# Optimization experiments

Hardware: AMD Instinct MI355X
Metric: run time of the kernel (lower is better)

The kernel has to match this reference:

```python
import jax, jax.numpy as jnp
import numpy as np

QMIN, QMAX = 0, 255        # 8-bit asymmetric activation quant bounds
GROUP_SIZE = 128

def setup_inputs() -> dict:
    key = jax.random.key(0)
    k1, k2, k3, k4, k5 = jax.random.split(key, 5)
    x = jax.random.normal(k1, (1, 2048, 4096), dtype=jnp.float32)
    qweight = jax.random.randint(k2, (4096, 32, 128), 0, 16, dtype=jnp.int32)  # uint4 codes
    w_scales = jax.random.uniform(k3, (4096, 32), dtype=jnp.float32, minval=0.001, maxval=0.02)
    w_zero_points = jax.random.randint(k4, (4096, 32), 0, 16, dtype=jnp.int32)
    bias = jax.random.normal(k5, (4096,), dtype=jnp.float32)
    return {"x": x, "qweight": qweight, "w_scales": w_scales,
            "w_zero_points": w_zero_points, "bias": bias}

def reference(x, qweight, w_scales, w_zero_points, bias):
    xf = x.astype(jnp.float32)
    # per-token (last-dim) asymmetric dynamic activation quantization
    xmin = jnp.min(xf, axis=-1, keepdims=True)
    xmax = jnp.max(xf, axis=-1, keepdims=True)
    x_scale = jnp.clip((xmax - xmin) / (QMAX - QMIN), 1e-5, None)
    x_zp = jnp.clip(jnp.round(-xmin / x_scale), QMIN, QMAX)
    q = jnp.clip(jnp.round(xf / x_scale) + x_zp, QMIN, QMAX)
    centered_x = (q - x_zp).reshape(*x.shape[:-1], -1, GROUP_SIZE)  # [B,S,G,C]
    # grouped weight dequant (zero-point centered)
    centered_w = qweight.astype(jnp.float32) - w_zero_points.astype(jnp.float32)[..., None]  # [O,G,C]
    acc = jnp.einsum('bsgc,ogc->bsog', centered_x, centered_w)  # [B,S,O,G]
    out = (acc * w_scales[None, None]).sum(axis=-1)  # apply per-group weight scales
    out = out * x_scale  # per-token activation scale
    out = out + bias
    return out
```

## Files before the change

kernel.cpp:

```cpp
#include <hip/hip_runtime.h>
#include <hip/hip_bf16.h>
#include <stdint.h>

#define M_DIM 2048
#define N_DIM 4096
#define K_DIM 4096
#define NGROUP 32
#define GSIZE 128

#define BM 128
#define BN 64
#define BKB 128

typedef __attribute__((ext_vector_type(4))) int   int32x4_t;
typedef __attribute__((ext_vector_type(4))) float f32x4_t;

static __device__ __forceinline__ void gl2lds16(const void* g, void* l) {
    auto gp = (const __attribute__((address_space(1))) unsigned int*)(uintptr_t)g;
    auto lp = (__attribute__((address_space(3))) unsigned int*)(uintptr_t)l;
    __builtin_amdgcn_global_load_lds(gp, lp, 16, 0, 0);
}

#define QUANT_BLOCKS M_DIM
#define DEQ_BLOCKS ((N_DIM * K_DIM) / 8 / 256)
#define WT_BLOCKS ((N_DIM * NGROUP) / 256)

__global__ __launch_bounds__(256) void prep_kernel(
        const float* __restrict__ x,
        const int* __restrict__ qw,
        const float* __restrict__ wsc,
        const int* __restrict__ wzp,
        char* __restrict__ A8,
        char* __restrict__ Bt8,
        float* __restrict__ xscale,
        float* __restrict__ xzpc,
        float* __restrict__ WS,
        float* __restrict__ wsct)
{
    const int t = threadIdx.x;
    if (blockIdx.x < QUANT_BLOCKS) {
        const int s = blockIdx.x;
        const float* xrow = x + (size_t)s * K_DIM;

        float xv[16];
        float vmin = 1e38f, vmax = -1e38f;
#pragma unroll
        for (int p = 0; p < 4; ++p) {
            float4 v = *((const float4*)(xrow + p * 1024) + t);
            xv[p*4+0] = v.x; xv[p*4+1] = v.y; xv[p*4+2] = v.z; xv[p*4+3] = v.w;
            vmin = fminf(vmin, fminf(fminf(v.x, v.y), fminf(v.z, v.w)));
            vmax = fmaxf(vmax, fmaxf(fmaxf(v.x, v.y), fmaxf(v.z, v.w)));
        }
#pragma unroll
        for (int off = 32; off > 0; off >>= 1) {
            vmin = fminf(vmin, __shfl_xor(vmin, off));
            vmax = fmaxf(vmax, __shfl_xor(vmax, off));
        }
        __shared__ float smin[4], smax[4];
        const int wave = t >> 6;
        if ((t & 63) == 0) { smin[wave] = vmin; smax[wave] = vmax; }
        __syncthreads();
        vmin = fminf(fminf(smin[0], smin[1]), fminf(smin[2], smin[3]));
        vmax = fmaxf(fmaxf(smax[0], smax[1]), fmaxf(smax[2], smax[3]));

        float sc = (vmax - vmin) / 255.0f;
        sc = fmaxf(sc, 1e-5f);
        float zp = rintf(-vmin / sc);
        zp = fminf(fmaxf(zp, 0.0f), 255.0f);

#pragma unroll
        for (int p = 0; p < 4; ++p) {
            int b[4];
#pragma unroll
            for (int e = 0; e < 4; ++e) {
                float q = fminf(fmaxf(rintf(xv[p*4+e] / sc) + zp, 0.0f), 255.0f);
                b[e] = (int)q - 128;
            }
            unsigned pack = (b[0] & 0xff) | ((b[1] & 0xff) << 8) |
                            ((b[2] & 0xff) << 16) | ((b[3] & 0xff) << 24);
            *(unsigned*)(A8 + (size_t)s * K_DIM + p * 1024 + t * 4) = pack;
        }
        if (t == 0) { xscale[s] = sc; xzpc[s] = 128.0f - zp; }
    } else if (blockIdx.x < QUANT_BLOCKS + DEQ_BLOCKS) {
        const size_t base = ((size_t)(blockIdx.x - QUANT_BLOCKS) * 256 + t) * 8;
        const int n = (int)(base >> 12);
        const int g = (int)((base >> 7) & 31);
        const int zp = wzp[n * NGROUP + g];

        int4 c0 = *(const int4*)(qw + base);
        int4 c1 = *(const int4*)(qw + base + 4);
        int v0 = c0.x - zp, v1 = c0.y - zp, v2 = c0.z - zp, v3 = c0.w - zp;
        int v4 = c1.x - zp, v5 = c1.y - zp, v6 = c1.z - zp, v7 = c1.w - zp;
        uint2 pk;
        pk.x = (v0 & 0xff) | ((v1 & 0xff) << 8) | ((v2 & 0xff) << 16) | ((v3 & 0xff) << 24);
        pk.y = (v4 & 0xff) | ((v5 & 0xff) << 8) | ((v6 & 0xff) << 16) | ((v7 & 0xff) << 24);
        *(uint2*)(Bt8 + base) = pk;

        int s8 = v0 + v1 + v2 + v3 + v4 + v5 + v6 + v7;
#pragma unroll
        for (int off = 1; off < 16; off <<= 1) s8 += __shfl_xor(s8, off);
        if ((t & 15) == 0)
            atomicAdd(WS + n, wsc[n * NGROUP + g] * (float)s8);
    } else {
        const int idx = (blockIdx.x - QUANT_BLOCKS - DEQ_BLOCKS) * 256 + t;
        const int n = idx >> 5, g = idx & 31;
        wsct[g * N_DIM + n] = wsc[idx];
    }
}

__global__ __launch_bounds__(256, 4) void gemm_kernel(
        const char* __restrict__ A8,
        const char* __restrict__ Bt8,
        const float* __restrict__ xscale,
        const float* __restrict__ xzpc,
        const float* __restrict__ wsct,
        const float* __restrict__ WS,
        const float* __restrict__ bias,
        float* __restrict__ out)
{
    __shared__ __align__(16) char As[BM * BKB];
    __shared__ __align__(16) char Bs[BN * BKB];

    const int tid  = threadIdx.x;
    const int bm   = blockIdx.y;
    const int bn   = blockIdx.x;
    const int wave = tid >> 6;
    const int lane = tid & 63;
    const int wr   = (wave >> 1) * 64;
    const int wc   = (wave & 1) * 32;
    const int lrow  = lane & 15;
    const int lquad = lane >> 4;
    const int l7    = lrow & 7;

    const int srow8 = lane >> 3;
    const int cdat  = (lane & 7) ^ srow8;

    int32x4_t iacc[4][2];
    f32x4_t   facc[4][2];
    const int32x4_t zi = {0, 0, 0, 0};
    const f32x4_t   zf = {0.f, 0.f, 0.f, 0.f};
#pragma unroll
    for (int i = 0; i < 4; ++i)
#pragma unroll
        for (int j = 0; j < 2; ++j) { iacc[i][j] = zi; facc[i][j] = zf; }

    const char* Ab = A8  + (size_t)(bm * BM) * K_DIM;
    const char* Bb = Bt8 + (size_t)(bn * BN) * K_DIM;

    for (int kt = 0; kt < K_DIM / GSIZE; ++kt) {
        const int k0 = kt * GSIZE;
        __syncthreads();
#pragma unroll
        for (int p = 0; p < 4; ++p) {
            const int rbase = (p * 4 + wave) * 8;
            gl2lds16(Ab + (size_t)(rbase + srow8) * K_DIM + k0 + cdat * 16,
                     As + rbase * BKB);
        }
#pragma unroll
        for (int p = 0; p < 2; ++p) {
            const int rbase = (p * 4 + wave) * 8;
            gl2lds16(Bb + (size_t)(rbase + srow8) * K_DIM + k0 + cdat * 16,
                     Bs + rbase * BKB);
        }
        __syncthreads();

#pragma unroll
        for (int ks = 0; ks < 2; ++ks) {
            const int kc = ks * 4 + lquad;
            int32x4_t af[4], bf[2];
#pragma unroll
            for (int i = 0; i < 4; ++i)
                af[i] = *(const int32x4_t*)(As + (wr + i * 16 + lrow) * BKB + ((kc ^ l7) * 16));
#pragma unroll
            for (int j = 0; j < 2; ++j)
                bf[j] = *(const int32x4_t*)(Bs + (wc + j * 16 + lrow) * BKB + ((kc ^ l7) * 16));
#pragma unroll
            for (int i = 0; i < 4; ++i)
#pragma unroll
                for (int j = 0; j < 2; ++j)
                    iacc[i][j] = __builtin_amdgcn_mfma_i32_16x16x64_i8(
                        af[i], bf[j], iacc[i][j], 0, 0, 0);
        }

#pragma unroll
        for (int j = 0; j < 2; ++j) {
            const int n = bn * BN + wc + j * 16 + lrow;
            const float scl = wsct[kt * N_DIM + n];
#pragma unroll
            for (int i = 0; i < 4; ++i) {
#pragma unroll
                for (int r = 0; r < 4; ++r)
                    facc[i][j][r] += scl * (float)iacc[i][j][r];
                iacc[i][j] = zi;
            }
        }
    }

    const int m0 = bm * BM + wr;
    const int n0 = bn * BN + wc;
    float wsn[2], bn2[2];
#pragma unroll
    for (int j = 0; j < 2; ++j) {
        const int n = n0 + j * 16 + lrow;
        wsn[j] = WS[n]; bn2[j] = bias[n];
    }
#pragma unroll
    for (int i = 0; i < 4; ++i) {
#pragma unroll
        for (int r = 0; r < 4; ++r) {
            const int m = m0 + i * 16 + lquad * 4 + r;
            const float xs = xscale[m];
            const float czp = xzpc[m];
#pragma unroll
            for (int j = 0; j < 2; ++j) {
                const int n = n0 + j * 16 + lrow;
                out[(size_t)m * N_DIM + n] = xs * (facc[i][j][r] + czp * wsn[j]) + bn2[j];
            }
        }
    }
}

extern "C" void kernel_launch(void* const* d_in, const int* in_sizes, int n_in,
                              void* d_out, int out_size, void* d_ws, size_t ws_size,
                              hipStream_t stream) {
    const float* x     = (const float*)d_in[0];
    const int*   qw    = (const int*)d_in[1];
    const float* wsc   = (const float*)d_in[2];
    const int*   wzp   = (const int*)d_in[3];
    const float* bias  = (const float*)d_in[4];
    float* out = (float*)d_out;

    char* A8  = (char*)d_ws;
    char* Bt8 = A8 + (size_t)M_DIM * K_DIM;
    float* xscale = (float*)(Bt8 + (size_t)N_DIM * K_DIM);
    float* xzpc   = xscale + M_DIM;
    float* WS     = xzpc + M_DIM;
    float* wsct   = WS + N_DIM;

    hipMemsetAsync(WS, 0, N_DIM * sizeof(float), stream);
    prep_kernel<<<QUANT_BLOCKS + DEQ_BLOCKS + WT_BLOCKS, 256, 0, stream>>>(
        x, qw, wsc, wzp, A8, Bt8, xscale, xzpc, WS, wsct);
    dim3 grid(N_DIM / BN, M_DIM / BM);
    gemm_kernel<<<grid, 256, 0, stream>>>(A8, Bt8, xscale, xzpc, wsct, WS, bias, out);
}
```

Measured before the change: 202.0 us.

## Enlarge GEMM tile to 128x128x256 with 32x32 int8 MFMA and LDS scales

```diff
diff --git a/kernel.cpp b/kernel.cpp
--- a/kernel.cpp
+++ b/kernel.cpp
@@ -9,11 +9,12 @@
 #define GSIZE 128
 
 #define BM 128
-#define BN 64
-#define BKB 128
-
-typedef __attribute__((ext_vector_type(4))) int   int32x4_t;
-typedef __attribute__((ext_vector_type(4))) float f32x4_t;
+#define BN 128
+#define BKB 256
+
+typedef __attribute__((ext_vector_type(4)))  int   int32x4_t;
+typedef __attribute__((ext_vector_type(16))) int   int32x16_t;
+typedef __attribute__((ext_vector_type(16))) float f32x16_t;
 
 static __device__ __forceinline__ void gl2lds16(const void* g, void* l) {
     auto gp = (const __attribute__((address_space(1))) unsigned int*)(uintptr_t)g;
@@ -23,7 +24,6 @@
 
 #define QUANT_BLOCKS M_DIM
 #define DEQ_BLOCKS ((N_DIM * K_DIM) / 8 / 256)
-#define WT_BLOCKS ((N_DIM * NGROUP) / 256)
 
 __global__ __launch_bounds__(256) void prep_kernel(
         const float* __restrict__ x,
@@ -34,8 +34,7 @@
         char* __restrict__ Bt8,
         float* __restrict__ xscale,
         float* __restrict__ xzpc,
-        float* __restrict__ WS,
-        float* __restrict__ wsct)
+        float* __restrict__ WS)
 {
     const int t = threadIdx.x;
     if (blockIdx.x < QUANT_BLOCKS) {
@@ -81,7 +80,7 @@
             *(unsigned*)(A8 + (size_t)s * K_DIM + p * 1024 + t * 4) = pack;
         }
         if (t == 0) { xscale[s] = sc; xzpc[s] = 128.0f - zp; }
-    } else if (blockIdx.x < QUANT_BLOCKS + DEQ_BLOCKS) {
+    } else {
         const size_t base = ((size_t)(blockIdx.x - QUANT_BLOCKS) * 256 + t) * 8;
         const int n = (int)(base >> 12);
         const int g = (int)((base >> 7) & 31);
@@ -101,25 +100,22 @@
         for (int off = 1; off < 16; off <<= 1) s8 += __shfl_xor(s8, off);
         if ((t & 15) == 0)
             atomicAdd(WS + n, wsc[n * NGROUP + g] * (float)s8);
-    } else {
-        const int idx = (blockIdx.x - QUANT_BLOCKS - DEQ_BLOCKS) * 256 + t;
-        const int n = idx >> 5, g = idx & 31;
-        wsct[g * N_DIM + n] = wsc[idx];
-    }
-}
-
-__global__ __launch_bounds__(256, 4) void gemm_kernel(
+    }
+}
+
+__global__ __launch_bounds__(256, 2) void gemm_kernel(
         const char* __restrict__ A8,
         const char* __restrict__ Bt8,
         const float* __restrict__ xscale,
         const float* __restrict__ xzpc,
-        const float* __restrict__ wsct,
+        const float* __restrict__ wsc,
         const float* __restrict__ WS,
         const float* __restrict__ bias,
         float* __restrict__ out)
 {
     __shared__ __align__(16) char As[BM * BKB];
     __shared__ __align__(16) char Bs[BN * BKB];
+    __shared__ float Ssc[NGROUP * BN];
 
     const int tid  = threadIdx.x;
     const int bm   = blockIdx.y;
@@ -127,94 +123,107 @@
     const int wave = tid >> 6;
     const int lane = tid & 63;
     const int wr   = (wave >> 1) * 64;
-    const int wc   = (wave & 1) * 32;
-    const int lrow  = lane & 15;
-    const int lquad = lane >> 4;
-    const int l7    = lrow & 7;
-
-    const int srow8 = lane >> 3;
-    const int cdat  = (lane & 7) ^ srow8;
-
-    int32x4_t iacc[4][2];
-    f32x4_t   facc[4][2];
-    const int32x4_t zi = {0, 0, 0, 0};
-    const f32x4_t   zf = {0.f, 0.f, 0.f, 0.f};
-#pragma unroll
-    for (int i = 0; i < 4; ++i)
-#pragma unroll
-        for (int j = 0; j < 2; ++j) { iacc[i][j] = zi; facc[i][j] = zf; }
+    const int wc   = (wave & 1) * 64;
+    const int l31  = lane & 31;
+    const int hi   = lane >> 5;
+    const int l7   = l31 & 7;
+
+    const int n0 = bn * BN;
+    {
+        const int n = tid >> 1, gh = (tid & 1) * 16;
+        const float4* src = (const float4*)(wsc + (size_t)(n0 + n) * NGROUP + gh);
+#pragma unroll
+        for (int j4 = 0; j4 < 4; ++j4) {
+            float4 v = src[j4];
+            Ssc[(gh + j4 * 4 + 0) * BN + n] = v.x;
+            Ssc[(gh + j4 * 4 + 1) * BN + n] = v.y;
+            Ssc[(gh + j4 * 4 + 2) * BN + n] = v.z;
+            Ssc[(gh + j4 * 4 + 3) * BN + n] = v.w;
+        }
+    }
+
+    int32x16_t iacc[2][2];
+    f32x16_t   facc[2][2];
+    int32x16_t ZERO;
+#pragma unroll
+    for (int r = 0; r < 16; ++r) ZERO[r] = 0;
+#pragma unroll
+    for (int i = 0; i < 2; ++i)
+#pragma unroll
+        for (int j = 0; j < 2; ++j) {
+            iacc[i][j] = ZERO;
+#pragma unroll
+            for (int r = 0; r < 16; ++r) facc[i][j][r] = 0.0f;
+        }
 
     const char* Ab = A8  + (size_t)(bm * BM) * K_DIM;
     const char* Bb = Bt8 + (size_t)(bn * BN) * K_DIM;
 
-    for (int kt = 0; kt < K_DIM / GSIZE; ++kt) {
-        const int k0 = kt * GSIZE;
+    const int srow4 = lane >> 4;
+
+    for (int kt = 0; kt < K_DIM / BKB; ++kt) {
+        const int k0 = kt * BKB;
         __syncthreads();
 #pragma unroll
-        for (int p = 0; p < 4; ++p) {
-            const int rbase = (p * 4 + wave) * 8;
-            gl2lds16(Ab + (size_t)(rbase + srow8) * K_DIM + k0 + cdat * 16,
-                     As + rbase * BKB);
-        }
-#pragma unroll
-        for (int p = 0; p < 2; ++p) {
-            const int rbase = (p * 4 + wave) * 8;
-            gl2lds16(Bb + (size_t)(rbase + srow8) * K_DIM + k0 + cdat * 16,
-                     Bs + rbase * BKB);
+        for (int p = 0; p < 8; ++p) {
+            const int rbase = (p * 4 + wave) * 4;
+            const int r = rbase + srow4;
+            const int cdat = (lane & 15) ^ (r & 7);
+            gl2lds16(Ab + (size_t)r * K_DIM + k0 + cdat * 16, As + rbase * BKB);
+            gl2lds16(Bb + (size_t)r * K_DIM + k0 + cdat * 16, Bs + rbase * BKB);
         }
         __syncthreads();
 
 #pragma unroll
-        for (int ks = 0; ks < 2; ++ks) {
-            const int kc = ks * 4 + lquad;
-            int32x4_t af[4], bf[2];
-#pragma unroll
-            for (int i = 0; i < 4; ++i)
-                af[i] = *(const int32x4_t*)(As + (wr + i * 16 + lrow) * BKB + ((kc ^ l7) * 16));
-#pragma unroll
-            for (int j = 0; j < 2; ++j)
-                bf[j] = *(const int32x4_t*)(Bs + (wc + j * 16 + lrow) * BKB + ((kc ^ l7) * 16));
-#pragma unroll
-            for (int i = 0; i < 4; ++i)
+        for (int half = 0; half < 2; ++half) {
+            const int g = kt * 2 + half;
+            float scl[2];
+            scl[0] = Ssc[g * BN + wc + 0  + l31];
+            scl[1] = Ssc[g * BN + wc + 32 + l31];
+
+#pragma unroll
+            for (int ks4 = 0; ks4 < 4; ++ks4) {
+                const int ks = half * 4 + ks4;
+                const int cc = ks * 2 + hi;
+                int32x4_t af[2], bf[2];
+#pragma unroll
+                for (int i = 0; i < 2; ++i)
+                    af[i] = *(const int32x4_t*)(As + (wr + i * 32 + l31) * BKB + ((cc ^ l7) * 16));
 #pragma unroll
                 for (int j = 0; j < 2; ++j)
-                    iacc[i][j] = __builtin_amdgcn_mfma_i32_16x16x64_i8(
-                        af[i], bf[j], iacc[i][j], 0, 0, 0);
-        }
-
-#pragma unroll
-        for (int j = 0; j < 2; ++j) {
-            const int n = bn * BN + wc + j * 16 + lrow;
-            const float scl = wsct[kt * N_DIM + n];
-#pragma unroll
-            for (int i = 0; i < 4; ++i) {
-#pragma unroll
-                for (int r = 0; r < 4; ++r)
-                    facc[i][j][r] += scl * (float)iacc[i][j][r];
-                iacc[i][j] = zi;
+                    bf[j] = *(const int32x4_t*)(Bs + (wc + j * 32 + l31) * BKB + ((cc ^ l7) * 16));
+#pragma unroll
+                for (int i = 0; i < 2; ++i)
+#pragma unroll
+                    for (int j = 0; j < 2; ++j)
+                        iacc[i][j] = __builtin_amdgcn_mfma_i32_32x32x32_i8(
+                            af[i], bf[j], ks4 == 0 ? ZERO : iacc[i][j], 0, 0, 0);
             }
+
+#pragma unroll
+            for (int i = 0; i < 2; ++i)
+#pragma unroll
+                for (int j = 0; j < 2; ++j)
+#pragma unroll
+                    for (int r = 0; r < 16; ++r)
+                        facc[i][j][r] += scl[j] * (float)iacc[i][j][r];
         }
     }
 
     const int m0 = bm * BM + wr;
-    const int n0 = bn * BN + wc;
-    float wsn[2], bn2[2];
 #pragma unroll
     for (int j = 0; j < 2; ++j) {
-        const int n = n0 + j * 16 + lrow;
-        wsn[j] = WS[n]; bn2[j] = bias[n];
-    }
-#pragma unroll
-    for (int i = 0; i < 4; ++i) {
-#pragma unroll
-        for (int r = 0; r < 4; ++r) {
-            const int m = m0 + i * 16 + lquad * 4 + r;
-            const float xs = xscale[m];
-            const float czp = xzpc[m];
-#pragma unroll
-            for (int j = 0; j < 2; ++j) {
-                const int n = n0 + j * 16 + lrow;
-                out[(size_t)m * N_DIM + n] = xs * (facc[i][j][r] + czp * wsn[j]) + bn2[j];
+        const int n = n0 + wc + j * 32 + l31;
+        const float wsn = WS[n];
+        const float bb  = bias[n];
+#pragma unroll
+        for (int i = 0; i < 2; ++i) {
+#pragma unroll
+            for (int r = 0; r < 16; ++r) {
+                const int m = m0 + i * 32 + (r & 3) + 8 * (r >> 2) + 4 * hi;
+                const float xs  = xscale[m];
+                const float czp = xzpc[m];
+                out[(size_t)m * N_DIM + n] = xs * (facc[i][j][r] + czp * wsn) + bb;
             }
         }
     }
@@ -235,11 +244,10 @@
     float* xscale = (float*)(Bt8 + (size_t)N_DIM * K_DIM);
     float* xzpc   = xscale + M_DIM;
     float* WS     = xzpc + M_DIM;
-    float* wsct   = WS + N_DIM;
 
     hipMemsetAsync(WS, 0, N_DIM * sizeof(float), stream);
-    prep_kernel<<<QUANT_BLOCKS + DEQ_BLOCKS + WT_BLOCKS, 256, 0, stream>>>(
-        x, qw, wsc, wzp, A8, Bt8, xscale, xzpc, WS, wsct);
+    prep_kernel<<<QUANT_BLOCKS + DEQ_BLOCKS, 256, 0, stream>>>(
+        x, qw, wsc, wzp, A8, Bt8, xscale, xzpc, WS);
     dim3 grid(N_DIM / BN, M_DIM / BM);
-    gemm_kernel<<<grid, 256, 0, stream>>>(A8, Bt8, xscale, xzpc, wsct, WS, bias, out);
-}
+    gemm_kernel<<<grid, 256, 0, stream>>>(A8, Bt8, xscale, xzpc, wsc, WS, bias, out);
+}
```

New measurement: 221.2 us. 9.5% more time.

## Enlarge GEMM tile to 128x128 and stage two quant groups per K step

Applied to the files above, without the earlier changes.

```diff
diff --git a/kernel.cpp b/kernel.cpp
--- a/kernel.cpp
+++ b/kernel.cpp
@@ -9,8 +9,8 @@
 #define GSIZE 128
 
 #define BM 128
-#define BN 64
-#define BKB 128
+#define BN 128
+#define BKB 256
 
 typedef __attribute__((ext_vector_type(4))) int   int32x4_t;
 typedef __attribute__((ext_vector_type(4))) float f32x4_t;
@@ -108,7 +108,7 @@
     }
 }
 
-__global__ __launch_bounds__(256, 4) void gemm_kernel(
+__global__ __launch_bounds__(256, 2) void gemm_kernel(
         const char* __restrict__ A8,
         const char* __restrict__ Bt8,
         const float* __restrict__ xscale,
@@ -127,94 +127,100 @@
     const int wave = tid >> 6;
     const int lane = tid & 63;
     const int wr   = (wave >> 1) * 64;
-    const int wc   = (wave & 1) * 32;
+    const int wc   = (wave & 1) * 64;
     const int lrow  = lane & 15;
     const int lquad = lane >> 4;
     const int l7    = lrow & 7;
 
-    const int srow8 = lane >> 3;
-    const int cdat  = (lane & 7) ^ srow8;
-
-    int32x4_t iacc[4][2];
-    f32x4_t   facc[4][2];
+    const int srow4 = lane >> 4;
+
+    int32x4_t iacc[4][4];
+    f32x4_t   facc[4][4];
     const int32x4_t zi = {0, 0, 0, 0};
-    const f32x4_t   zf = {0.f, 0.f, 0.f, 0.f};
 #pragma unroll
     for (int i = 0; i < 4; ++i)
 #pragma unroll
-        for (int j = 0; j < 2; ++j) { iacc[i][j] = zi; facc[i][j] = zf; }
+        for (int j = 0; j < 4; ++j) {
+            iacc[i][j] = zi;
+            facc[i][j] = (f32x4_t){0.f, 0.f, 0.f, 0.f};
+        }
 
     const char* Ab = A8  + (size_t)(bm * BM) * K_DIM;
     const char* Bb = Bt8 + (size_t)(bn * BN) * K_DIM;
-
-    for (int kt = 0; kt < K_DIM / GSIZE; ++kt) {
-        const int k0 = kt * GSIZE;
+    const int n0 = bn * BN;
+
+    for (int kt = 0; kt < K_DIM / BKB; ++kt) {
+        const int k0 = kt * BKB;
+        const int g0 = kt * 2;
+
+        float scl0[4], scl1[4];
+#pragma unroll
+        for (int j = 0; j < 4; ++j) {
+            const int n = n0 + wc + j * 16 + lrow;
+            scl0[j] = wsct[g0 * N_DIM + n];
+            scl1[j] = wsct[(g0 + 1) * N_DIM + n];
+        }
+
         __syncthreads();
 #pragma unroll
-        for (int p = 0; p < 4; ++p) {
-            const int rbase = (p * 4 + wave) * 8;
-            gl2lds16(Ab + (size_t)(rbase + srow8) * K_DIM + k0 + cdat * 16,
-                     As + rbase * BKB);
-        }
-#pragma unroll
-        for (int p = 0; p < 2; ++p) {
-            const int rbase = (p * 4 + wave) * 8;
-            gl2lds16(Bb + (size_t)(rbase + srow8) * K_DIM + k0 + cdat * 16,
-                     Bs + rbase * BKB);
+        for (int p = 0; p < 8; ++p) {
+            const int rbase = (p * 4 + wave) * 4;
+            const int r = rbase + srow4;
+            const int cdat = (lane & 15) ^ (r & 7);
+            gl2lds16(Ab + (size_t)r * K_DIM + k0 + cdat * 16, As + rbase * BKB);
+            gl2lds16(Bb + (size_t)r * K_DIM + k0 + cdat * 16, Bs + rbase * BKB);
         }
         __syncthreads();
 
 #pragma unroll
-        for (int ks = 0; ks < 2; ++ks) {
+        for (int ks = 0; ks < 4; ++ks) {
             const int kc = ks * 4 + lquad;
-            int32x4_t af[4], bf[2];
+            int32x4_t af[4], bf[4];
 #pragma unroll
             for (int i = 0; i < 4; ++i)
                 af[i] = *(const int32x4_t*)(As + (wr + i * 16 + lrow) * BKB + ((kc ^ l7) * 16));
 #pragma unroll
-            for (int j = 0; j < 2; ++j)
+            for (int j = 0; j < 4; ++j)
                 bf[j] = *(const int32x4_t*)(Bs + (wc + j * 16 + lrow) * BKB + ((kc ^ l7) * 16));
+            const bool first = (ks & 1) == 0;
 #pragma unroll
             for (int i = 0; i < 4; ++i)
 #pragma unroll
-                for (int j = 0; j < 2; ++j)
+                for (int j = 0; j < 4; ++j)
                     iacc[i][j] = __builtin_amdgcn_mfma_i32_16x16x64_i8(
-                        af[i], bf[j], iacc[i][j], 0, 0, 0);
-        }
-
-#pragma unroll
-        for (int j = 0; j < 2; ++j) {
-            const int n = bn * BN + wc + j * 16 + lrow;
-            const float scl = wsct[kt * N_DIM + n];
-#pragma unroll
-            for (int i = 0; i < 4; ++i) {
-#pragma unroll
-                for (int r = 0; r < 4; ++r)
-                    facc[i][j][r] += scl * (float)iacc[i][j][r];
-                iacc[i][j] = zi;
+                        af[i], bf[j], first ? zi : iacc[i][j], 0, 0, 0);
+
+            if (ks & 1) {
+                const float* scl = (ks == 1) ? scl0 : scl1;
+#pragma unroll
+                for (int j = 0; j < 4; ++j)
+#pragma unroll
+                    for (int i = 0; i < 4; ++i)
+#pragma unroll
+                        for (int r = 0; r < 4; ++r)
+                            facc[i][j][r] += scl[j] * (float)iacc[i][j][r];
             }
         }
     }
 
     const int m0 = bm * BM + wr;
-    const int n0 = bn * BN + wc;
-    float wsn[2], bn2[2];
-#pragma unroll
-    for (int j = 0; j < 2; ++j) {
-        const int n = n0 + j * 16 + lrow;
-        wsn[j] = WS[n]; bn2[j] = bias[n];
+    float wsn[4], bb[4];
+#pragma unroll
+    for (int j = 0; j < 4; ++j) {
+        const int n = n0 + wc + j * 16 + lrow;
+        wsn[j] = WS[n]; bb[j] = bias[n];
     }
 #pragma unroll
     for (int i = 0; i < 4; ++i) {
 #pragma unroll
         for (int r = 0; r < 4; ++r) {
             const int m = m0 + i * 16 + lquad * 4 + r;
-            const float xs = xscale[m];
+            const float xs  = xscale[m];
             const float czp = xzpc[m];
 #pragma unroll
-            for (int j = 0; j < 2; ++j) {
-                const int n = n0 + j * 16 + lrow;
-                out[(size_t)m * N_DIM + n] = xs * (facc[i][j][r] + czp * wsn[j]) + bn2[j];
+            for (int j = 0; j < 4; ++j) {
+                const int n = n0 + wc + j * 16 + lrow;
+                out[(size_t)m * N_DIM + n] = xs * (facc[i][j][r] + czp * wsn[j]) + bb[j];
             }
         }
     }
```

Result: slower. 237.3 us (+17.5%).

## Double-buffer LDS tiles in int8 GEMM and replace float atomics with reduction kernel

Applied to the files above, without the earlier changes.

```diff
diff --git a/kernel.cpp b/kernel.cpp
--- a/kernel.cpp
+++ b/kernel.cpp
@@ -34,7 +34,7 @@
         char* __restrict__ Bt8,
         float* __restrict__ xscale,
         float* __restrict__ xzpc,
-        float* __restrict__ WS,
+        int* __restrict__ Sw,
         float* __restrict__ wsct)
 {
     const int t = threadIdx.x;
@@ -100,7 +100,7 @@
 #pragma unroll
         for (int off = 1; off < 16; off <<= 1) s8 += __shfl_xor(s8, off);
         if ((t & 15) == 0)
-            atomicAdd(WS + n, wsc[n * NGROUP + g] * (float)s8);
+            Sw[n * NGROUP + g] = s8;
     } else {
         const int idx = (blockIdx.x - QUANT_BLOCKS - DEQ_BLOCKS) * 256 + t;
         const int n = idx >> 5, g = idx & 31;
@@ -108,7 +108,24 @@
     }
 }
 
-__global__ __launch_bounds__(256, 4) void gemm_kernel(
+__global__ __launch_bounds__(256) void ws_kernel(
+        const float* __restrict__ wsc, const int* __restrict__ Sw,
+        float* __restrict__ WS)
+{
+    const int n = blockIdx.x * 256 + threadIdx.x;
+    const float4* w4 = (const float4*)(wsc + n * NGROUP);
+    const int4*   s4 = (const int4*)(Sw + n * NGROUP);
+    float acc = 0.f;
+#pragma unroll
+    for (int p = 0; p < 8; ++p) {
+        float4 w = w4[p]; int4 s = s4[p];
+        acc += w.x * (float)s.x + w.y * (float)s.y +
+               w.z * (float)s.z + w.w * (float)s.w;
+    }
+    WS[n] = acc;
+}
+
+__global__ __launch_bounds__(256, 3) void gemm_kernel(
         const char* __restrict__ A8,
         const char* __restrict__ Bt8,
         const float* __restrict__ xscale,
@@ -118,8 +135,8 @@
         const float* __restrict__ bias,
         float* __restrict__ out)
 {
-    __shared__ __align__(16) char As[BM * BKB];
-    __shared__ __align__(16) char Bs[BN * BKB];
+    __shared__ __align__(16) char As[2][BM * BKB];
+    __shared__ __align__(16) char Bs[2][BN * BKB];
 
     const int tid  = threadIdx.x;
     const int bm   = blockIdx.y;
@@ -138,31 +155,59 @@
     int32x4_t iacc[4][2];
     f32x4_t   facc[4][2];
     const int32x4_t zi = {0, 0, 0, 0};
-    const f32x4_t   zf = {0.f, 0.f, 0.f, 0.f};
 #pragma unroll
     for (int i = 0; i < 4; ++i)
 #pragma unroll
-        for (int j = 0; j < 2; ++j) { iacc[i][j] = zi; facc[i][j] = zf; }
+        for (int j = 0; j < 2; ++j) {
+            iacc[i][j] = zi;
+            facc[i][j] = (f32x4_t){0.f, 0.f, 0.f, 0.f};
+        }
 
     const char* Ab = A8  + (size_t)(bm * BM) * K_DIM;
     const char* Bb = Bt8 + (size_t)(bn * BN) * K_DIM;
+    const int n0 = bn * BN;
+    const int ncol0 = n0 + wc + 0  + lrow;
+    const int ncol1 = n0 + wc + 16 + lrow;
+
+#pragma unroll
+    for (int p = 0; p < 4; ++p) {
+        const int rbase = (p * 4 + wave) * 8;
+        gl2lds16(Ab + (size_t)(rbase + srow8) * K_DIM + cdat * 16,
+                 As[0] + rbase * BKB);
+    }
+#pragma unroll
+    for (int p = 0; p < 2; ++p) {
+        const int rbase = (p * 4 + wave) * 8;
+        gl2lds16(Bb + (size_t)(rbase + srow8) * K_DIM + cdat * 16,
+                 Bs[0] + rbase * BKB);
+    }
+    float scl0 = wsct[ncol0];
+    float scl1 = wsct[ncol1];
 
     for (int kt = 0; kt < K_DIM / GSIZE; ++kt) {
-        const int k0 = kt * GSIZE;
+        const int cur = kt & 1;
         __syncthreads();
-#pragma unroll
-        for (int p = 0; p < 4; ++p) {
-            const int rbase = (p * 4 + wave) * 8;
-            gl2lds16(Ab + (size_t)(rbase + srow8) * K_DIM + k0 + cdat * 16,
-                     As + rbase * BKB);
-        }
-#pragma unroll
-        for (int p = 0; p < 2; ++p) {
-            const int rbase = (p * 4 + wave) * 8;
-            gl2lds16(Bb + (size_t)(rbase + srow8) * K_DIM + k0 + cdat * 16,
-                     Bs + rbase * BKB);
-        }
-        __syncthreads();
+
+        if (kt < 31) {
+            const int k0 = (kt + 1) * GSIZE;
+#pragma unroll
+            for (int p = 0; p < 4; ++p) {
+                const int rbase = (p * 4 + wave) * 8;
+                gl2lds16(Ab + (size_t)(rbase + srow8) * K_DIM + k0 + cdat * 16,
+                         As[cur ^ 1] + rbase * BKB);
+            }
+#pragma unroll
+            for (int p = 0; p < 2; ++p) {
+                const int rbase = (p * 4 + wave) * 8;
+                gl2lds16(Bb + (size_t)(rbase + srow8) * K_DIM + k0 + cdat * 16,
+                         Bs[cur ^ 1] + rbase * BKB);
+            }
+        }
+        float nscl0 = 0.f, nscl1 = 0.f;
+        if (kt < 31) {
+            nscl0 = wsct[(kt + 1) * N_DIM + ncol0];
+            nscl1 = wsct[(kt + 1) * N_DIM + ncol1];
+        }
 
 #pragma unroll
         for (int ks = 0; ks < 2; ++ks) {
@@ -170,52 +215,41 @@
             int32x4_t af[4], bf[2];
 #pragma unroll
             for (int i = 0; i < 4; ++i)
-                af[i] = *(const int32x4_t*)(As + (wr + i * 16 + lrow) * BKB + ((kc ^ l7) * 16));
+                af[i] = *(const int32x4_t*)(As[cur] + (wr + i * 16 + lrow) * BKB + ((kc ^ l7) * 16));
 #pragma unroll
             for (int j = 0; j < 2; ++j)
-                bf[j] = *(const int32x4_t*)(Bs + (wc + j * 16 + lrow) * BKB + ((kc ^ l7) * 16));
+                bf[j] = *(const int32x4_t*)(Bs[cur] + (wc + j * 16 + lrow) * BKB + ((kc ^ l7) * 16));
 #pragma unroll
             for (int i = 0; i < 4; ++i)
 #pragma unroll
                 for (int j = 0; j < 2; ++j)
                     iacc[i][j] = __builtin_amdgcn_mfma_i32_16x16x64_i8(
-                        af[i], bf[j], iacc[i][j], 0, 0, 0);
-        }
-
-#pragma unroll
-        for (int j = 0; j < 2; ++j) {
-            const int n = bn * BN + wc + j * 16 + lrow;
-            const float scl = wsct[kt * N_DIM + n];
-#pragma unroll
-            for (int i = 0; i < 4; ++i) {
-#pragma unroll
-                for (int r = 0; r < 4; ++r)
-                    facc[i][j][r] += scl * (float)iacc[i][j][r];
-                iacc[i][j] = zi;
-            }
-        }
+                        af[i], bf[j], ks == 0 ? zi : iacc[i][j], 0, 0, 0);
+        }
+
+#pragma unroll
+        for (int i = 0; i < 4; ++i) {
+#pragma unroll
+            for (int r = 0; r < 4; ++r) {
+                facc[i][0][r] += scl0 * (float)iacc[i][0][r];
+                facc[i][1][r] += scl1 * (float)iacc[i][1][r];
+            }
+        }
+        scl0 = nscl0; scl1 = nscl1;
     }
 
     const int m0 = bm * BM + wr;
-    const int n0 = bn * BN + wc;
-    float wsn[2], bn2[2];
-#pragma unroll
-    for (int j = 0; j < 2; ++j) {
-        const int n = n0 + j * 16 + lrow;
-        wsn[j] = WS[n]; bn2[j] = bias[n];
-    }
+    const float wsn0 = WS[ncol0], bb0 = bias[ncol0];
+    const float wsn1 = WS[ncol1], bb1 = bias[ncol1];
 #pragma unroll
     for (int i = 0; i < 4; ++i) {
 #pragma unroll
         for (int r = 0; r < 4; ++r) {
             const int m = m0 + i * 16 + lquad * 4 + r;
-            const float xs = xscale[m];
+            const float xs  = xscale[m];
             const float czp = xzpc[m];
-#pragma unroll
-            for (int j = 0; j < 2; ++j) {
-                const int n = n0 + j * 16 + lrow;
-                out[(size_t)m * N_DIM + n] = xs * (facc[i][j][r] + czp * wsn[j]) + bn2[j];
-            }
+            out[(size_t)m * N_DIM + ncol0] = xs * (facc[i][0][r] + czp * wsn0) + bb0;
+            out[(size_t)m * N_DIM + ncol1] = xs * (facc[i][1][r] + czp * wsn1) + bb1;
         }
     }
 }
@@ -235,11 +269,12 @@
     float* xscale = (float*)(Bt8 + (size_t)N_DIM * K_DIM);
     float* xzpc   = xscale + M_DIM;
     float* WS     = xzpc + M_DIM;
-    float* wsct   = WS + N_DIM;
-
-    hipMemsetAsync(WS, 0, N_DIM * sizeof(float), stream);
+    int*   Sw     = (int*)(WS + N_DIM);
+    float* wsct   = (float*)(Sw + N_DIM * NGROUP);
+
     prep_kernel<<<QUANT_BLOCKS + DEQ_BLOCKS + WT_BLOCKS, 256, 0, stream>>>(
-        x, qw, wsc, wzp, A8, Bt8, xscale, xzpc, WS, wsct);
+        x, qw, wsc, wzp, A8, Bt8, xscale, xzpc, Sw, wsct);
+    ws_kernel<<<N_DIM / 256, 256, 0, stream>>>(wsc, Sw, WS);
     dim3 grid(N_DIM / BN, M_DIM / BM);
     gemm_kernel<<<grid, 256, 0, stream>>>(A8, Bt8, xscale, xzpc, wsct, WS, bias, out);
 }
```

New measurement: 182.1 us. -9.9%, faster.
